# Kernel optimization log

Measured on AMD Instinct MI355X. Metric: run time of the kernel, lower is better.

The kernel has to match this reference:

```python
import jax, jax.numpy as jnp
import numpy as np

# Topology constants (fixed DAG ontology)
B = 16384          # batch
IN_DIM = 4096      # input_dim
N_LEAF = 64        # leaf terms with direct input maps
IPL = 64           # inputs per leaf (disjoint slices; one-hot connection mask -> diag weights)
N_MID = 16         # mid-level modules
CPM = 4            # leaf children per mid module
MID_N = 128        # neurons per mid module
OUT = 256          # output_dim at root


def setup_inputs() -> dict:
    key = jax.random.key(0)
    k = jax.random.split(key, 7)
    return {
        "x": jax.random.normal(k[0], (B, IN_DIM), jnp.float32),
        # input-layer kernels: only the masked diagonal entries of each [IN_DIM, IPL]
        # kernel are nonzero after kernel*connections, so store them as [N_LEAF, IPL]
        "w_inp": jax.random.normal(k[1], (N_LEAF, IPL), jnp.float32) * 0.1,
        "pbias": jnp.ones((N_LEAF,), jnp.float32),  # pbias=1.0 per input layer
        "W_mid": jax.random.normal(k[2], (N_MID, CPM * IPL, MID_N), jnp.float32) * 0.05,
        "b_mid": jnp.zeros((N_MID, MID_N), jnp.float32),
        "W_root": jax.random.normal(k[3], (N_MID * MID_N, OUT), jnp.float32) * 0.05,
        "b_root": jnp.zeros((OUT,), jnp.float32),
    }


def reference(x, w_inp, pbias, W_mid, b_mid, W_root, b_root):
    b = x.shape[0]
    # Leaf input layers: gather each leaf's input slice, multiply by its diagonal
    # kernel entries (== dot(x, kernel*one_hot_mask)), linear act, add pbias.
    leaf = x.reshape(b, N_LEAF, IPL) * w_inp + pbias[:, None]          # [B, N_LEAF, IPL]
    # Mid modules: concat CPM leaf children -> masked-dense (mask all ones) + bias + tanh
    mid_in = leaf.reshape(b, N_MID, CPM * IPL)                          # [B, N_MID, 256]
    mid = jnp.tanh(jnp.einsum('bgi,gio->bgo', mid_in, W_mid) + b_mid)   # [B, N_MID, 128]
    # Root module: concat all mid children -> dense + bias, linear output activation
    out = mid.reshape(b, N_MID * MID_N) @ W_root + b_root               # [B, OUT]
    return out
```

## Files before the change

### kernel.cpp

```cpp
#include <hip/hip_runtime.h>

typedef __attribute__((ext_vector_type(8))) short short8;
typedef __attribute__((ext_vector_type(4))) float floatx4;
typedef unsigned short ushort_t;
typedef unsigned int uint32;


__device__ __forceinline__ uint32 f2bf_bits(float f) {
  uint32 u = __builtin_bit_cast(uint32, f);
  u += 0x7fffu + ((u >> 16) & 1u);
  return u >> 16;
}

__device__ __forceinline__ float tanh_fast(float x) {
  float e = __expf(2.0f * x);
  return 1.0f - 2.0f * __builtin_amdgcn_rcpf(e + 1.0f);
}

#define MFMA16(a, b, c) __builtin_amdgcn_mfma_f32_16x16x32_bf16((a), (b), (c), 0, 0, 0)


__global__ __launch_bounds__(256) void prep(const float* __restrict__ w_inp,
                                            const float* __restrict__ pbias,
                                            const float* __restrict__ W_mid,
                                            const float* __restrict__ b_mid,
                                            const float* __restrict__ W_root,
                                            ushort_t* __restrict__ Wtm,
                                            ushort_t* __restrict__ Wtr,
                                            float* __restrict__ bias_eff) {
  const int b = blockIdx.x, t = threadIdx.x;
  if (b < 2048) {
    const int idx = b * 256 + t;
    const int g = idx >> 15;
    const int rem = idx & 32767;
    const int i = rem >> 7;
    const int o = rem & 127;
    const float v = W_mid[(g << 15) + i * 128 + o] * w_inp[g * 256 + i];
    Wtm[(g << 15) + o * 256 + i] = (ushort_t)f2bf_bits(v);
  } else if (b < 4096) {
    const int idx = (b - 2048) * 256 + t;
    const int k = idx >> 8;
    const int o = idx & 255;
    Wtr[o * 2048 + k] = (ushort_t)f2bf_bits(W_root[k * 256 + o]);
  } else {
    const int g = b - 4096;
    const int o = t;
    if (o < 128) {
      float s = b_mid[g * 128 + o];
      const float* wp = W_mid + (g << 15) + o;
      float pb[4];
#pragma unroll
      for (int q = 0; q < 4; ++q) pb[q] = pbias[g * 4 + q];
#pragma unroll 8
      for (int i = 0; i < 256; ++i) s += pb[i >> 6] * wp[i * 128];
      bias_eff[g * 128 + o] = s;
    }
  }
}


__global__ __launch_bounds__(256) void fused(const float* __restrict__ x,
                                             const ushort_t* __restrict__ Wtm,
                                             const ushort_t* __restrict__ Wtr,
                                             const float* __restrict__ bias_eff,
                                             const float* __restrict__ b_root,
                                             float* __restrict__ out) {
  __shared__ __align__(16) ushort_t sX[32 * 264];
  __shared__ __align__(16) ushort_t sMid[32 * 136];

  const int t = threadIdx.x;
  const int lane = t & 63;
  const int wv = __builtin_amdgcn_readfirstlane(t >> 6);
  const int m0 = blockIdx.x * 32;
  const int l15 = lane & 15;
  const int kh = lane >> 4;

  const int xr = t >> 3, xq = t & 7;
  const float* xbase = x + (size_t)(m0 + xr) * 4096 + xq * 4;
  uint32* sxw = (uint32*)(sX + xr * 264 + xq * 4);

  const ushort_t* sxa0 = sX + l15 * 264 + kh * 8;
  const ushort_t* sxa1 = sX + (16 + l15) * 264 + kh * 8;
  const ushort_t* sma0 = sMid + l15 * 136 + kh * 8;
  const ushort_t* sma1 = sMid + (16 + l15) * 136 + kh * 8;

  const ushort_t* wtm_b0 = Wtm + (wv * 32 + l15) * 256 + kh * 8;
  const ushort_t* wtm_b1 = Wtm + (wv * 32 + 16 + l15) * 256 + kh * 8;
  const ushort_t* wtr_b  = Wtr + (wv * 64 + l15) * 2048 + kh * 8;

  float4 rx[8];
  floatx4 racc[2][4] = {};

#pragma unroll
  for (int p = 0; p < 8; ++p) rx[p] = *(const float4*)(xbase + p * 32);

  for (int g = 0; g < 16; ++g) {
    __syncthreads();

#pragma unroll
    for (int p = 0; p < 8; ++p) {
      uint32 bx = __builtin_bit_cast(uint32, rx[p].x) + 0x8000u;
      uint32 by = __builtin_bit_cast(uint32, rx[p].y) + 0x8000u;
      uint32 bz = __builtin_bit_cast(uint32, rx[p].z) + 0x8000u;
      uint32 bw = __builtin_bit_cast(uint32, rx[p].w) + 0x8000u;
      uint32 lo = __builtin_amdgcn_perm(by, bx, 0x07060302u);
      uint32 hi = __builtin_amdgcn_perm(bw, bz, 0x07060302u);
      *(uint2*)(sxw + p * 16) = make_uint2(lo, hi);
    }

    const ushort_t* wb0 = wtm_b0 + (g << 15);
    const ushort_t* wb1 = wtm_b1 + (g << 15);
    short8 mb[2][2];
    mb[0][0] = *(const short8*)(wb0);
    mb[0][1] = *(const short8*)(wb1);
    mb[1][0] = *(const short8*)(wb0 + 32);
    mb[1][1] = *(const short8*)(wb1 + 32);

    {
      const float* xn = xbase + (g < 15 ? g + 1 : 15) * 256;
#pragma unroll
      for (int p = 0; p < 8; ++p) rx[p] = *(const float4*)(xn + p * 32);
    }

    const float bias0 = bias_eff[g * 128 + wv * 32 + l15];
    const float bias1 = bias_eff[g * 128 + wv * 32 + 16 + l15];

    __syncthreads();

    floatx4 macc[2][2] = {};
#pragma unroll
    for (int kk = 0; kk < 8; ++kk) {
      short8 a0 = *(const short8*)(sxa0 + kk * 32);
      short8 a1 = *(const short8*)(sxa1 + kk * 32);
      short8 b0 = mb[kk & 1][0], b1 = mb[kk & 1][1];
      const int kn = (kk + 2 <= 7) ? kk + 2 : 7;
      mb[kk & 1][0] = *(const short8*)(wb0 + kn * 32);
      mb[kk & 1][1] = *(const short8*)(wb1 + kn * 32);
      macc[0][0] = MFMA16(a0, b0, macc[0][0]);
      macc[0][1] = MFMA16(a0, b1, macc[0][1]);
      macc[1][0] = MFMA16(a1, b0, macc[1][0]);
      macc[1][1] = MFMA16(a1, b1, macc[1][1]);
    }

#pragma unroll
    for (int ni = 0; ni < 2; ++ni) {
      const float bias = ni ? bias1 : bias0;
      const int col = wv * 32 + ni * 16 + l15;
#pragma unroll
      for (int mi = 0; mi < 2; ++mi)
#pragma unroll
        for (int r = 0; r < 4; ++r) {
          const int row = mi * 16 + kh * 4 + r;
          sMid[row * 136 + col] = (ushort_t)f2bf_bits(tanh_fast(macc[mi][ni][r] + bias));
        }
    }

    const ushort_t* wb = wtr_b + g * 128;
    short8 rb[2][4];
#pragma unroll
    for (int ni = 0; ni < 4; ++ni) rb[0][ni] = *(const short8*)(wb + ni * 16 * 2048);
#pragma unroll
    for (int ni = 0; ni < 4; ++ni) rb[1][ni] = *(const short8*)(wb + ni * 16 * 2048 + 32);

    __syncthreads();

#pragma unroll
    for (int kk2 = 0; kk2 < 4; ++kk2) {
      short8 a0 = *(const short8*)(sma0 + kk2 * 32);
      short8 a1 = *(const short8*)(sma1 + kk2 * 32);
      short8 b0 = rb[kk2 & 1][0], b1 = rb[kk2 & 1][1];
      short8 b2 = rb[kk2 & 1][2], b3 = rb[kk2 & 1][3];
      const int kn = (kk2 + 2 <= 3) ? kk2 + 2 : 3;
#pragma unroll
      for (int ni = 0; ni < 4; ++ni)
        rb[kk2 & 1][ni] = *(const short8*)(wb + ni * 16 * 2048 + kn * 32);
      racc[0][0] = MFMA16(a0, b0, racc[0][0]);
      racc[0][1] = MFMA16(a0, b1, racc[0][1]);
      racc[0][2] = MFMA16(a0, b2, racc[0][2]);
      racc[0][3] = MFMA16(a0, b3, racc[0][3]);
      racc[1][0] = MFMA16(a1, b0, racc[1][0]);
      racc[1][1] = MFMA16(a1, b1, racc[1][1]);
      racc[1][2] = MFMA16(a1, b2, racc[1][2]);
      racc[1][3] = MFMA16(a1, b3, racc[1][3]);
    }
  }

#pragma unroll
  for (int ni = 0; ni < 4; ++ni) {
    const int col = wv * 64 + ni * 16 + l15;
    const float br = b_root[col];
#pragma unroll
    for (int mi = 0; mi < 2; ++mi)
#pragma unroll
      for (int r = 0; r < 4; ++r) {
        const int row = m0 + mi * 16 + kh * 4 + r;
        out[row * 256 + col] = racc[mi][ni][r] + br;
      }
  }
}


extern "C" void kernel_launch(void* const* d_in, const int* in_sizes, int n_in,
                              void* d_out, int out_size, void* d_ws, size_t ws_size,
                              hipStream_t stream) {
  const float* x      = (const float*)d_in[0];
  const float* w_inp  = (const float*)d_in[1];
  const float* pbias  = (const float*)d_in[2];
  const float* W_mid  = (const float*)d_in[3];
  const float* b_mid  = (const float*)d_in[4];
  const float* W_root = (const float*)d_in[5];
  const float* b_root = (const float*)d_in[6];
  float* out = (float*)d_out;

  char* ws = (char*)d_ws;
  ushort_t* Wtm      = (ushort_t*)(ws);
  ushort_t* Wtr      = (ushort_t*)(ws + (1 << 20));
  float*    bias_eff = (float*)   (ws + (2 << 20));

  prep<<<dim3(4112), dim3(256), 0, stream>>>(w_inp, pbias, W_mid, b_mid, W_root, Wtm, Wtr, bias_eff);
  fused<<<dim3(512), dim3(256), 0, stream>>>(x, Wtm, Wtr, bias_eff, b_root, out);
}
```

Before: 451.4 us.

## Split-K fused kernel across mid groups, tile prep transposes, restructure barriers

The prep kernel now transposes weights through 32x32 shared-memory tiles for coalesced reads and writes, and splits the bias reduction across two thread halves. The fused kernel can split the 16 mid groups across two blocks per row tile, doubling the grid from 512 to 1024 blocks. Partial outputs go to a workspace buffer and a separate reduction kernel adds them with the root bias. It also cuts one barrier per iteration, replaces __syncthreads with a raw lgkmcnt wait plus s_barrier, reorders x prefetch and root-weight loads with sched barriers, and sets occupancy launch bounds. In exchange, the split path writes and rereads two full fp32 partial outputs and adds a third launch, and it depends on the workspace being large enough.

```diff
diff --git a/kernel.cpp b/kernel.cpp
--- a/kernel.cpp
+++ b/kernel.cpp
@@ -18,6 +18,8 @@
 }
 
 #define MFMA16(a, b, c) __builtin_amdgcn_mfma_f32_16x16x32_bf16((a), (b), (c), 0, 0, 0)
+
+#define BAR_LGKM() asm volatile("s_waitcnt lgkmcnt(0)\n\ts_barrier" ::: "memory")
 
 
 __global__ __launch_bounds__(256) void prep(const float* __restrict__ w_inp,
@@ -28,55 +30,79 @@
                                             ushort_t* __restrict__ Wtm,
                                             ushort_t* __restrict__ Wtr,
                                             float* __restrict__ bias_eff) {
+  __shared__ float tl[32][33];
+  __shared__ float red[256];
   const int b = blockIdx.x, t = threadIdx.x;
-  if (b < 2048) {
-    const int idx = b * 256 + t;
-    const int g = idx >> 15;
-    const int rem = idx & 32767;
-    const int i = rem >> 7;
-    const int o = rem & 127;
-    const float v = W_mid[(g << 15) + i * 128 + o] * w_inp[g * 256 + i];
-    Wtm[(g << 15) + o * 256 + i] = (ushort_t)f2bf_bits(v);
-  } else if (b < 4096) {
-    const int idx = (b - 2048) * 256 + t;
-    const int k = idx >> 8;
-    const int o = idx & 255;
-    Wtr[o * 2048 + k] = (ushort_t)f2bf_bits(W_root[k * 256 + o]);
+  const int tx = t & 31, ty = t >> 5;
+
+  if (b < 512) {
+    const int g = b >> 5, tile = b & 31;
+    const int i0 = (tile >> 2) * 32, o0 = (tile & 3) * 32;
+#pragma unroll
+    for (int r = 0; r < 4; ++r) {
+      const int il = ty * 4 + r;
+      tl[il][tx] = W_mid[(g << 15) + (i0 + il) * 128 + o0 + tx] * w_inp[g * 256 + i0 + il];
+    }
+    __syncthreads();
+#pragma unroll
+    for (int r = 0; r < 4; ++r) {
+      const int orow = ty * 4 + r;
+      Wtm[(g << 15) + (o0 + orow) * 256 + i0 + tx] = (ushort_t)f2bf_bits(tl[tx][orow]);
+    }
+  } else if (b < 1024) {
+    const int bb = b - 512;
+    const int k0 = (bb >> 3) * 32, o0 = (bb & 7) * 32;
+#pragma unroll
+    for (int r = 0; r < 4; ++r) {
+      const int kl = ty * 4 + r;
+      tl[kl][tx] = W_root[(k0 + kl) * 256 + o0 + tx];
+    }
+    __syncthreads();
+#pragma unroll
+    for (int r = 0; r < 4; ++r) {
+      const int orow = ty * 4 + r;
+      Wtr[(o0 + orow) * 2048 + k0 + tx] = (ushort_t)f2bf_bits(tl[tx][orow]);
+    }
   } else {
-    const int g = b - 4096;
-    const int o = t;
-    if (o < 128) {
-      float s = b_mid[g * 128 + o];
-      const float* wp = W_mid + (g << 15) + o;
-      float pb[4];
-#pragma unroll
-      for (int q = 0; q < 4; ++q) pb[q] = pbias[g * 4 + q];
+    const int g = b - 1024;
+    const int o = t & 127, ih = t >> 7;
+    const float* wp = W_mid + (g << 15) + ih * 128 * 128 + o;
+    const float pb0 = pbias[g * 4 + ih * 2];
+    const float pb1 = pbias[g * 4 + ih * 2 + 1];
+    float s = 0.f;
 #pragma unroll 8
-      for (int i = 0; i < 256; ++i) s += pb[i >> 6] * wp[i * 128];
-      bias_eff[g * 128 + o] = s;
-    }
-  }
-}
-
-
-__global__ __launch_bounds__(256) void fused(const float* __restrict__ x,
-                                             const ushort_t* __restrict__ Wtm,
-                                             const ushort_t* __restrict__ Wtr,
-                                             const float* __restrict__ bias_eff,
-                                             const float* __restrict__ b_root,
-                                             float* __restrict__ out) {
+    for (int ii = 0; ii < 128; ++ii) s += (ii < 64 ? pb0 : pb1) * wp[ii * 128];
+    red[t] = s;
+    __syncthreads();
+    if (ih == 0) bias_eff[g * 128 + o] = b_mid[g * 128 + o] + red[o] + red[128 + o];
+  }
+}
+
+
+template <bool SPLIT>
+__global__ __launch_bounds__(256, 3) void fused(const float* __restrict__ x,
+                                                const ushort_t* __restrict__ Wtm,
+                                                const ushort_t* __restrict__ Wtr,
+                                                const float* __restrict__ bias_eff,
+                                                const float* __restrict__ b_root,
+                                                float* __restrict__ dst) {
+  constexpr int GROUPS = SPLIT ? 8 : 16;
+
   __shared__ __align__(16) ushort_t sX[32 * 264];
   __shared__ __align__(16) ushort_t sMid[32 * 136];
 
   const int t = threadIdx.x;
   const int lane = t & 63;
   const int wv = __builtin_amdgcn_readfirstlane(t >> 6);
-  const int m0 = blockIdx.x * 32;
+  const int tile = SPLIT ? (int)(blockIdx.x >> 1) : (int)blockIdx.x;
+  const int h = SPLIT ? (int)(blockIdx.x & 1) : 0;
+  const int G0 = h * 8;
+  const int m0 = tile * 32;
   const int l15 = lane & 15;
   const int kh = lane >> 4;
 
   const int xr = t >> 3, xq = t & 7;
-  const float* xbase = x + (size_t)(m0 + xr) * 4096 + xq * 4;
+  const float* xbase = x + (size_t)(m0 + xr) * 4096 + (size_t)G0 * 256 + xq * 4;
   uint32* sxw = (uint32*)(sX + xr * 264 + xq * 4);
 
   const ushort_t* sxa0 = sX + l15 * 264 + kh * 8;
@@ -84,9 +110,9 @@
   const ushort_t* sma0 = sMid + l15 * 136 + kh * 8;
   const ushort_t* sma1 = sMid + (16 + l15) * 136 + kh * 8;
 
-  const ushort_t* wtm_b0 = Wtm + (wv * 32 + l15) * 256 + kh * 8;
-  const ushort_t* wtm_b1 = Wtm + (wv * 32 + 16 + l15) * 256 + kh * 8;
-  const ushort_t* wtr_b  = Wtr + (wv * 64 + l15) * 2048 + kh * 8;
+  const ushort_t* wtm_b0 = Wtm + ((size_t)G0 << 15) + (wv * 32 + l15) * 256 + kh * 8;
+  const ushort_t* wtm_b1 = wtm_b0 + 16 * 256;
+  const ushort_t* wtr_b = Wtr + (wv * 64 + l15) * 2048 + (size_t)G0 * 128 + kh * 8;
 
   float4 rx[8];
   floatx4 racc[2][4] = {};
@@ -94,8 +120,17 @@
 #pragma unroll
   for (int p = 0; p < 8; ++p) rx[p] = *(const float4*)(xbase + p * 32);
 
-  for (int g = 0; g < 16; ++g) {
-    __syncthreads();
+#pragma unroll 1
+  for (int g = 0; g < GROUPS; ++g) {
+    const ushort_t* wb0 = wtm_b0 + ((size_t)g << 15);
+    const ushort_t* wb1 = wtm_b1 + ((size_t)g << 15);
+    short8 mb[2][2];
+    mb[0][0] = *(const short8*)(wb0);
+    mb[0][1] = *(const short8*)(wb1);
+    mb[1][0] = *(const short8*)(wb0 + 32);
+    mb[1][1] = *(const short8*)(wb1 + 32);
+    const float bias0 = bias_eff[(G0 + g) * 128 + wv * 32 + l15];
+    const float bias1 = bias_eff[(G0 + g) * 128 + wv * 32 + 16 + l15];
 
 #pragma unroll
     for (int p = 0; p < 8; ++p) {
@@ -108,24 +143,7 @@
       *(uint2*)(sxw + p * 16) = make_uint2(lo, hi);
     }
 
-    const ushort_t* wb0 = wtm_b0 + (g << 15);
-    const ushort_t* wb1 = wtm_b1 + (g << 15);
-    short8 mb[2][2];
-    mb[0][0] = *(const short8*)(wb0);
-    mb[0][1] = *(const short8*)(wb1);
-    mb[1][0] = *(const short8*)(wb0 + 32);
-    mb[1][1] = *(const short8*)(wb1 + 32);
-
-    {
-      const float* xn = xbase + (g < 15 ? g + 1 : 15) * 256;
-#pragma unroll
-      for (int p = 0; p < 8; ++p) rx[p] = *(const float4*)(xn + p * 32);
-    }
-
-    const float bias0 = bias_eff[g * 128 + wv * 32 + l15];
-    const float bias1 = bias_eff[g * 128 + wv * 32 + 16 + l15];
-
-    __syncthreads();
+    BAR_LGKM();
 
     floatx4 macc[2][2] = {};
 #pragma unroll
@@ -133,15 +151,33 @@
       short8 a0 = *(const short8*)(sxa0 + kk * 32);
       short8 a1 = *(const short8*)(sxa1 + kk * 32);
       short8 b0 = mb[kk & 1][0], b1 = mb[kk & 1][1];
-      const int kn = (kk + 2 <= 7) ? kk + 2 : 7;
-      mb[kk & 1][0] = *(const short8*)(wb0 + kn * 32);
-      mb[kk & 1][1] = *(const short8*)(wb1 + kn * 32);
+      if (kk < 6) {
+        mb[kk & 1][0] = *(const short8*)(wb0 + (kk + 2) * 32);
+        mb[kk & 1][1] = *(const short8*)(wb1 + (kk + 2) * 32);
+      }
       macc[0][0] = MFMA16(a0, b0, macc[0][0]);
       macc[0][1] = MFMA16(a0, b1, macc[0][1]);
       macc[1][0] = MFMA16(a1, b0, macc[1][0]);
       macc[1][1] = MFMA16(a1, b1, macc[1][1]);
     }
 
+    const ushort_t* wb = wtr_b + g * 128;
+    short8 rb[2][4];
+#pragma unroll
+    for (int ni = 0; ni < 4; ++ni) rb[0][ni] = *(const short8*)(wb + ni * 16 * 2048);
+#pragma unroll
+    for (int ni = 0; ni < 4; ++ni) rb[1][ni] = *(const short8*)(wb + ni * 16 * 2048 + 32);
+
+    __builtin_amdgcn_sched_barrier(0);
+
+    if (g < GROUPS - 1) {
+      const float* xn = xbase + (g + 1) * 256;
+#pragma unroll
+      for (int p = 0; p < 8; ++p) rx[p] = *(const float4*)(xn + p * 32);
+    }
+
+    __builtin_amdgcn_sched_barrier(0);
+
 #pragma unroll
     for (int ni = 0; ni < 2; ++ni) {
       const float bias = ni ? bias1 : bias0;
@@ -155,14 +191,7 @@
         }
     }
 
-    const ushort_t* wb = wtr_b + g * 128;
-    short8 rb[2][4];
-#pragma unroll
-    for (int ni = 0; ni < 4; ++ni) rb[0][ni] = *(const short8*)(wb + ni * 16 * 2048);
-#pragma unroll
-    for (int ni = 0; ni < 4; ++ni) rb[1][ni] = *(const short8*)(wb + ni * 16 * 2048 + 32);
-
-    __syncthreads();
+    BAR_LGKM();
 
 #pragma unroll
     for (int kk2 = 0; kk2 < 4; ++kk2) {
@@ -170,10 +199,11 @@
       short8 a1 = *(const short8*)(sma1 + kk2 * 32);
       short8 b0 = rb[kk2 & 1][0], b1 = rb[kk2 & 1][1];
       short8 b2 = rb[kk2 & 1][2], b3 = rb[kk2 & 1][3];
-      const int kn = (kk2 + 2 <= 3) ? kk2 + 2 : 3;
-#pragma unroll
-      for (int ni = 0; ni < 4; ++ni)
-        rb[kk2 & 1][ni] = *(const short8*)(wb + ni * 16 * 2048 + kn * 32);
+      if (kk2 < 2) {
+#pragma unroll
+        for (int ni = 0; ni < 4; ++ni)
+          rb[kk2 & 1][ni] = *(const short8*)(wb + ni * 16 * 2048 + (kk2 + 2) * 32);
+      }
       racc[0][0] = MFMA16(a0, b0, racc[0][0]);
       racc[0][1] = MFMA16(a0, b1, racc[0][1]);
       racc[0][2] = MFMA16(a0, b2, racc[0][2]);
@@ -185,18 +215,35 @@
     }
   }
 
+  float* o = SPLIT ? dst + (size_t)h * (16384 * 256) : dst;
 #pragma unroll
   for (int ni = 0; ni < 4; ++ni) {
     const int col = wv * 64 + ni * 16 + l15;
-    const float br = b_root[col];
+    const float br = SPLIT ? 0.0f : b_root[col];
 #pragma unroll
     for (int mi = 0; mi < 2; ++mi)
 #pragma unroll
       for (int r = 0; r < 4; ++r) {
         const int row = m0 + mi * 16 + kh * 4 + r;
-        out[row * 256 + col] = racc[mi][ni][r] + br;
+        o[(size_t)row * 256 + col] = racc[mi][ni][r] + br;
       }
   }
+}
+
+
+__global__ __launch_bounds__(256) void reducek(const float* __restrict__ part,
+                                               const float* __restrict__ b_root,
+                                               float* __restrict__ out) {
+  const int i = blockIdx.x * 256 + threadIdx.x;
+  float4 a = ((const float4*)part)[i];
+  float4 c = ((const float4*)(part + (size_t)16384 * 256))[i];
+  float4 br = ((const float4*)b_root)[i & 63];
+  float4 r;
+  r.x = a.x + c.x + br.x;
+  r.y = a.y + c.y + br.y;
+  r.z = a.z + c.z + br.z;
+  r.w = a.w + c.w + br.w;
+  ((float4*)out)[i] = r;
 }
 
 
@@ -216,7 +263,16 @@
   ushort_t* Wtm      = (ushort_t*)(ws);
   ushort_t* Wtr      = (ushort_t*)(ws + (1 << 20));
   float*    bias_eff = (float*)   (ws + (2 << 20));
-
-  prep<<<dim3(4112), dim3(256), 0, stream>>>(w_inp, pbias, W_mid, b_mid, W_root, Wtm, Wtr, bias_eff);
-  fused<<<dim3(512), dim3(256), 0, stream>>>(x, Wtm, Wtr, bias_eff, b_root, out);
-}
+  float*    part     = (float*)   (ws + (4 << 20));
+
+  const size_t need = (size_t)(4 << 20) + 2ull * 16384 * 256 * 4;
+  const bool split = ws_size >= need;
+
+  prep<<<dim3(1040), dim3(256), 0, stream>>>(w_inp, pbias, W_mid, b_mid, W_root, Wtm, Wtr, bias_eff);
+  if (split) {
+    fused<true><<<dim3(1024), dim3(256), 0, stream>>>(x, Wtm, Wtr, bias_eff, b_root, part);
+    reducek<<<dim3(4096), dim3(256), 0, stream>>>(part, b_root, out);
+  } else {
+    fused<false><<<dim3(512), dim3(256), 0, stream>>>(x, Wtm, Wtr, bias_eff, b_root, out);
+  }
+}
```

After: 449.1 us. About the same (-0.5%).
